# Kernel optimization log

Measured on AMD Instinct MI355X. Metric: run time of the kernel, lower is better.

## Reference

```python
import jax, jax.numpy as jnp
import numpy as np
from jax import lax

B, DIM, H, W = 8, 192, 128, 128
HEADS = 4
CH = DIM // HEADS            # per-head channels = 48
D_RED = max(DIM // 8, 4)     # SKFusion reduction dim = 24
HEIGHT = 2


def setup_inputs() -> dict:
    key = jax.random.key(0)
    ks = jax.random.split(key, 32)
    rn = lambda i, shp, s=1.0: jax.random.normal(ks[i], shp, jnp.float32) * s
    inp = {
        "T_E_input": rn(0, (B, DIM, H, W)),
        "C_E_input": rn(1, (B, DIM, H, W)),
        "T_D_input": rn(2, (B, DIM, H, W)),
        # LayerNorm2d params
        "tn_w": jnp.ones((DIM,), jnp.float32), "tn_b": jnp.zeros((DIM,), jnp.float32),
        "cn_w": jnp.ones((DIM,), jnp.float32), "cn_b": jnp.zeros((DIM,), jnp.float32),
        # Q/K/V: 1x1 conv [O,C] + depthwise 3x3 [DIM,1,3,3]
        "q_w": rn(3, (DIM, DIM), 0.05), "q_b": jnp.zeros((DIM,), jnp.float32),
        "q_dw": rn(4, (DIM, 1, 3, 3), 0.05), "q_db": jnp.zeros((DIM,), jnp.float32),
        "k_w": rn(5, (DIM, DIM), 0.05), "k_b": jnp.zeros((DIM,), jnp.float32),
        "k_dw": rn(6, (DIM, 1, 3, 3), 0.05), "k_db": jnp.zeros((DIM,), jnp.float32),
        "v_w": rn(7, (DIM, DIM), 0.05), "v_b": jnp.zeros((DIM,), jnp.float32),
        "v_dw": rn(8, (DIM, 1, 3, 3), 0.05), "v_db": jnp.zeros((DIM,), jnp.float32),
        "temperature": jnp.ones((1, 1, 1), jnp.float32),
        "proj_w": rn(9, (DIM, DIM), 0.05), "proj_b": jnp.zeros((DIM,), jnp.float32),
        "a1": jnp.full((1,), 0.2, jnp.float32),
        "a2": jnp.full((1,), 0.2, jnp.float32),
        "a3": jnp.full((1,), 0.2, jnp.float32),
        "a4": jnp.full((1,), 0.2, jnp.float32),
        # SKFusion mlp (both conv 1x1, no bias)
        "sk_w1": rn(10, (D_RED, DIM), 0.05),
        "sk_w2": rn(11, (DIM * HEIGHT, D_RED), 0.05),
    }
    return inp


def _ln2d(x, w, b, eps=1e-6):
    mu = x.mean(axis=1, keepdims=True)
    var = x.var(axis=1, keepdims=True)
    return (x - mu) / jnp.sqrt(var + eps) * w[None, :, None, None] + b[None, :, None, None]


def _conv1x1(x, w, b=None):
    y = jnp.einsum('bchw,oc->bohw', x, w)
    return y if b is None else y + b[None, :, None, None]


def _dwconv3x3(x, w, b):
    y = lax.conv_general_dilated(x, w, (1, 1), 'SAME',
                                 feature_group_count=DIM,
                                 dimension_numbers=('NCHW', 'OIHW', 'NCHW'))
    return y + b[None, :, None, None]


def _l2norm(x, eps=1e-12):
    n = jnp.sqrt(jnp.sum(x * x, axis=-1, keepdims=True))
    return x / jnp.maximum(n, eps)


def _topk_masked(attn, k):
    # mask built from top-k indices via scatter (one-hot over last axis)
    idx = lax.top_k(attn, k)[1]                              # [b,h,C,k]
    mask = jax.nn.one_hot(idx, attn.shape[-1], dtype=bool).any(axis=-2)
    return jnp.where(mask, attn, -jnp.inf)


def _gfm_forward(T_E_input, C_E_input, T_D_input,
                 tn_w, tn_b, cn_w, cn_b,
                 q_w, q_b, q_dw, q_db,
                 k_w, k_b, k_dw, k_db,
                 v_w, v_b, v_dw, v_db,
                 temperature, proj_w, proj_b,
                 a1, a2, a3, a4, sk_w1, sk_w2):
    b, c, h, w = T_E_input.shape
    T_E = _ln2d(T_E_input, tn_w, tn_b)
    C_E = _ln2d(C_E_input, cn_w, cn_b)

    q = _dwconv3x3(_conv1x1(T_E, q_w, q_b), q_dw, q_db)
    k = _dwconv3x3(_conv1x1(C_E, k_w, k_b), k_dw, k_db)
    v = _dwconv3x3(_conv1x1(C_E, v_w, v_b), v_dw, v_db)

    hw = h * w
    q = _l2norm(q.reshape(b, HEADS, CH, hw))   # normalize along token dim
    k = _l2norm(k.reshape(b, HEADS, CH, hw))
    v = v.reshape(b, HEADS, CH, hw)

    attn = jnp.einsum('bhcn,bhdn->bhcd', q, k) * temperature  # [b,h,C,C]

    C = CH
    ks = [C // 2, C * 2 // 3, int(C * 3 / 4), int(C * 4 / 5)]
    p1 = jax.nn.softmax(_topk_masked(attn, ks[0]), axis=-1)
    p2 = jax.nn.softmax(_topk_masked(attn, ks[1]), axis=-1)
    p3 = jax.nn.softmax(_topk_masked(attn, ks[2]), axis=-1)
    p4 = jax.nn.softmax(_topk_masked(attn, ks[3]), axis=-1)

    o1 = jnp.einsum('bhcd,bhdn->bhcn', p1, v)
    o2 = jnp.einsum('bhcd,bhdn->bhcn', p2, v)
    o3 = jnp.einsum('bhcd,bhdn->bhcn', p3, v)
    o4 = jnp.einsum('bhcd,bhdn->bhcn', p4, v)
    out = o1 * a1 + o2 * a2 + o3 * a3 + o4 * a4

    fusion1 = _conv1x1(out.reshape(b, c, h, w), proj_w, proj_b) + C_E_input

    # SKFusion over [fusion1, T_D_input]
    feats = jnp.stack([fusion1, T_D_input], axis=1)          # [b,2,c,h,w]
    feats_sum = feats.sum(axis=1)                            # [b,c,h,w]
    pooled = feats_sum.mean(axis=(2, 3), keepdims=True)      # [b,c,1,1]
    z = jax.nn.relu(_conv1x1(pooled, sk_w1))
    gate = _conv1x1(z, sk_w2).reshape(b, HEIGHT, c, 1, 1)
    gate = jax.nn.softmax(gate, axis=1)
    return (feats * gate).sum(axis=1)


def reference(T_E_input, C_E_input, T_D_input,
              tn_w, tn_b, cn_w, cn_b,
              q_w, q_b, q_dw, q_db,
              k_w, k_b, k_dw, k_db,
              v_w, v_b, v_dw, v_db,
              temperature, proj_w, proj_b,
              a1, a2, a3, a4, sk_w1, sk_w2):
    return _gfm_forward(T_E_input, C_E_input, T_D_input,
                        tn_w, tn_b, cn_w, cn_b,
                        q_w, q_b, q_dw, q_db,
                        k_w, k_b, k_dw, k_db,
                        v_w, v_b, v_dw, v_db,
                        temperature, proj_w, proj_b,
                        a1, a2, a3, a4, sk_w1, sk_w2)
```

## Files before the change

### kernel.cpp

```cpp
#include <hip/hip_runtime.h>
#include <hip/hip_bf16.h>

#define BATCH 8
#define CDIM 192
#define HH 128
#define WW 128
#define HW (HH*WW)
#define HEADS 4
#define CHD 48
#define NSL 64
#define LDK 40

typedef __attribute__((ext_vector_type(8))) short bf16x8;
typedef __attribute__((ext_vector_type(4))) float f32x4;

__device__ inline unsigned short f2bf(float f) {
    union { float f; unsigned int u; } v; v.f = f;
    unsigned int u = v.u;
    unsigned int r = u + 0x7fff + ((u >> 16) & 1);
    return (unsigned short)(r >> 16);
}

__global__ __launch_bounds__(256) void ln_part_kernel(
    const float* __restrict__ x, float* __restrict__ ps, float* __restrict__ ps2)
{
    const int idx = blockIdx.x * 256 + threadIdx.x;
    const int slice = blockIdx.y;
    const int b = idx >> 14;
    const int p = idx & (HW - 1);
    const float* xp = x + (size_t)b * CDIM * HW + (size_t)slice * 48 * HW + p;
    float s = 0.f, s2 = 0.f;
#pragma unroll 8
    for (int c = 0; c < 48; ++c) {
        float v = xp[(size_t)c * HW];
        s += v;
        s2 = fmaf(v, v, s2);
    }
    ps [slice * (BATCH * HW) + idx] = s;
    ps2[slice * (BATCH * HW) + idx] = s2;
}

__global__ __launch_bounds__(256) void ln_fin_kernel(
    const float* __restrict__ ps, const float* __restrict__ ps2,
    float* __restrict__ mu, float* __restrict__ rstd)
{
    const int idx = blockIdx.x * 256 + threadIdx.x;
    const int N = BATCH * HW;
    float s  = ps [idx] + ps [N + idx] + ps [2 * N + idx] + ps [3 * N + idx];
    float s2 = ps2[idx] + ps2[N + idx] + ps2[2 * N + idx] + ps2[3 * N + idx];
    float m = s * (1.f / CDIM);
    mu[idx] = m;
    rstd[idx] = rsqrtf(s2 * (1.f / CDIM) - m * m + 1e-6f);
}

__global__ __launch_bounds__(256) void rowsum_kernel(
    const float* __restrict__ x, float* __restrict__ out)
{
    const int row = blockIdx.x;
    const float4* xp = (const float4*)(x + (size_t)row * HW);
    float s = 0.f;
#pragma unroll
    for (int k = 0; k < 16; ++k) {
        float4 v = xp[threadIdx.x + k * 256];
        s += (v.x + v.y) + (v.z + v.w);
    }
    for (int msk = 32; msk; msk >>= 1) s += __shfl_xor(s, msk);
    __shared__ float sh[4];
    if ((threadIdx.x & 63) == 0) sh[threadIdx.x >> 6] = s;
    __syncthreads();
    if (threadIdx.x == 0) out[row] = sh[0] + sh[1] + sh[2] + sh[3];
}

__global__ __launch_bounds__(256) void conv1x1_mfma_ln(
    const float* __restrict__ x, const float* __restrict__ mu, const float* __restrict__ rstd,
    const float* __restrict__ lnw, const float* __restrict__ lnb,
    const float* __restrict__ w, const float* __restrict__ wb,
    float* __restrict__ y)
{
    __shared__ short A_s[CDIM * LDK];
    __shared__ short B_s[64 * LDK];
    const int tid = threadIdx.x;
    const int p0 = blockIdx.x * 64;
    const int b  = blockIdx.y;
    const int lane = tid & 63;
    const int wid = tid >> 6;
    const int p_l = tid & 63;

    const int sidx = (b << 14) + p0 + p_l;
    const float m_ln = mu[sidx], r_ln = rstd[sidx];

    f32x4 acc[12];
#pragma unroll
    for (int i = 0; i < 12; ++i) acc[i] = f32x4{0.f, 0.f, 0.f, 0.f};

    const size_t xb = (size_t)b * CDIM * HW + p0;

    for (int ks = 0; ks < 6; ++ks) {
        const int k0 = ks * 32;
        if (ks) __syncthreads();
#pragma unroll
        for (int j = 0; j < 3; ++j) {
            const int row = p_l + 64 * j;
#pragma unroll
            for (int i = 0; i < 2; ++i) {
                const int c = k0 + wid * 8 + i * 4;
                const float4 wv = *(const float4*)(w + (size_t)row * CDIM + c);
                unsigned int lo = f2bf(wv.x) | ((unsigned int)f2bf(wv.y) << 16);
                unsigned int hi = f2bf(wv.z) | ((unsigned int)f2bf(wv.w) << 16);
                *(uint2*)&A_s[row * LDK + wid * 8 + i * 4] = make_uint2(lo, hi);
            }
        }
#pragma unroll
        for (int i = 0; i < 2; ++i) {
            const int c = k0 + wid * 8 + i * 4;
            float v0 = x[xb + (size_t)(c + 0) * HW + p_l];
            float v1 = x[xb + (size_t)(c + 1) * HW + p_l];
            float v2 = x[xb + (size_t)(c + 2) * HW + p_l];
            float v3 = x[xb + (size_t)(c + 3) * HW + p_l];
            v0 = (v0 - m_ln) * r_ln * lnw[c + 0] + lnb[c + 0];
            v1 = (v1 - m_ln) * r_ln * lnw[c + 1] + lnb[c + 1];
            v2 = (v2 - m_ln) * r_ln * lnw[c + 2] + lnb[c + 2];
            v3 = (v3 - m_ln) * r_ln * lnw[c + 3] + lnb[c + 3];
            unsigned int lo = f2bf(v0) | ((unsigned int)f2bf(v1) << 16);
            unsigned int hi = f2bf(v2) | ((unsigned int)f2bf(v3) << 16);
            *(uint2*)&B_s[p_l * LDK + wid * 8 + i * 4] = make_uint2(lo, hi);
        }
        __syncthreads();
        const bf16x8 bfr = *(const bf16x8*)&B_s[(wid * 16 + (lane & 15)) * LDK + (lane >> 4) * 8];
#pragma unroll
        for (int mi = 0; mi < 12; ++mi) {
            const bf16x8 afr = *(const bf16x8*)&A_s[(mi * 16 + (lane & 15)) * LDK + (lane >> 4) * 8];
            acc[mi] = __builtin_amdgcn_mfma_f32_16x16x32_bf16(afr, bfr, acc[mi], 0, 0, 0);
        }
    }
    const int col = p0 + wid * 16 + (lane & 15);
#pragma unroll
    for (int mi = 0; mi < 12; ++mi) {
#pragma unroll
        for (int r = 0; r < 4; ++r) {
            const int row = mi * 16 + (lane >> 4) * 4 + r;
            y[((size_t)b * CDIM + row) * HW + col] = acc[mi][r] + wb[row];
        }
    }
}

__global__ __launch_bounds__(256) void projfuse_mfma(
    const float* __restrict__ v, const float* __restrict__ M,
    const float* __restrict__ pb, const float* __restrict__ resid,
    float* __restrict__ y)
{
    __shared__ short A_s[CDIM * LDK];
    __shared__ short B_s[64 * LDK];
    const int tid = threadIdx.x;
    const int p0 = blockIdx.x * 64;
    const int b  = blockIdx.y;
    const int lane = tid & 63;
    const int wid = tid >> 6;
    const int p_l = tid & 63;

    f32x4 acc[12];
#pragma unroll
    for (int i = 0; i < 12; ++i) acc[i] = f32x4{0.f, 0.f, 0.f, 0.f};

    const size_t xb = (size_t)b * CDIM * HW + p0;
    const float* Mb = M + (size_t)b * CDIM * CDIM;

    for (int ks = 0; ks < 6; ++ks) {
        const int k0 = ks * 32;
        if (ks) __syncthreads();
#pragma unroll
        for (int j = 0; j < 3; ++j) {
            const int row = p_l + 64 * j;
#pragma unroll
            for (int i = 0; i < 2; ++i) {
                const int c = k0 + wid * 8 + i * 4;
                const float4 wv = *(const float4*)(Mb + (size_t)row * CDIM + c);
                unsigned int lo = f2bf(wv.x) | ((unsigned int)f2bf(wv.y) << 16);
                unsigned int hi = f2bf(wv.z) | ((unsigned int)f2bf(wv.w) << 16);
                *(uint2*)&A_s[row * LDK + wid * 8 + i * 4] = make_uint2(lo, hi);
            }
        }
#pragma unroll
        for (int i = 0; i < 2; ++i) {
            const int c = k0 + wid * 8 + i * 4;
            float v0 = v[xb + (size_t)(c + 0) * HW + p_l];
            float v1 = v[xb + (size_t)(c + 1) * HW + p_l];
            float v2 = v[xb + (size_t)(c + 2) * HW + p_l];
            float v3 = v[xb + (size_t)(c + 3) * HW + p_l];
            unsigned int lo = f2bf(v0) | ((unsigned int)f2bf(v1) << 16);
            unsigned int hi = f2bf(v2) | ((unsigned int)f2bf(v3) << 16);
            *(uint2*)&B_s[p_l * LDK + wid * 8 + i * 4] = make_uint2(lo, hi);
        }
        __syncthreads();
        const bf16x8 bfr = *(const bf16x8*)&B_s[(wid * 16 + (lane & 15)) * LDK + (lane >> 4) * 8];
#pragma unroll
        for (int mi = 0; mi < 12; ++mi) {
            const bf16x8 afr = *(const bf16x8*)&A_s[(mi * 16 + (lane & 15)) * LDK + (lane >> 4) * 8];
            acc[mi] = __builtin_amdgcn_mfma_f32_16x16x32_bf16(afr, bfr, acc[mi], 0, 0, 0);
        }
    }
    const int col = p0 + wid * 16 + (lane & 15);
#pragma unroll
    for (int mi = 0; mi < 12; ++mi) {
#pragma unroll
        for (int r = 0; r < 4; ++r) {
            const int row = mi * 16 + (lane >> 4) * 4 + r;
            const size_t o = ((size_t)b * CDIM + row) * HW + col;
            y[o] = acc[mi][r] + pb[row] + resid[o];
        }
    }
}

__global__ __launch_bounds__(256) void dwconv_kernel(
    const float* __restrict__ x, const float* __restrict__ w, const float* __restrict__ bias,
    float* __restrict__ y, float* __restrict__ sumsq)
{
    const int rt = blockIdx.x, c = blockIdx.y, b = blockIdx.z;
    const int tid = threadIdx.x;
    const int lrow = tid >> 3;
    const int c16  = (tid & 7) * 16;
    const int gr = rt * 32 + lrow;
    const float* xp = x + ((size_t)b * CDIM + c) * HW;

    float wv[9];
#pragma unroll
    for (int t = 0; t < 9; ++t) wv[t] = w[c * 9 + t];
    const float bs = bias[c];

    float rb[3][24];
#pragma unroll
    for (int dr = 0; dr < 3; ++dr) {
        const int grr = gr + dr - 1;
        const bool ok = (grr >= 0) && (grr < HH);
        const float4* rp = (const float4*)(xp + (size_t)(ok ? grr : 0) * WW);
        float4 z = make_float4(0.f, 0.f, 0.f, 0.f);
        float4 t0 = (ok && c16 > 0)        ? rp[(c16 >> 2) - 1] : z;
        float4 t1 = ok ? rp[(c16 >> 2) + 0] : z;
        float4 t2 = ok ? rp[(c16 >> 2) + 1] : z;
        float4 t3 = ok ? rp[(c16 >> 2) + 2] : z;
        float4 t4 = ok ? rp[(c16 >> 2) + 3] : z;
        float4 t5 = (ok && c16 + 16 < WW)  ? rp[(c16 >> 2) + 4] : z;
        *(float4*)&rb[dr][0]  = t0;
        *(float4*)&rb[dr][4]  = t1;
        *(float4*)&rb[dr][8]  = t2;
        *(float4*)&rb[dr][12] = t3;
        *(float4*)&rb[dr][16] = t4;
        *(float4*)&rb[dr][20] = t5;
    }

    float out[16];
#pragma unroll
    for (int p = 0; p < 16; ++p) out[p] = bs;
#pragma unroll
    for (int dr = 0; dr < 3; ++dr) {
#pragma unroll
        for (int p = 0; p < 16; ++p) {
            out[p] = fmaf(wv[dr * 3 + 0], rb[dr][3 + p], out[p]);
            out[p] = fmaf(wv[dr * 3 + 1], rb[dr][4 + p], out[p]);
            out[p] = fmaf(wv[dr * 3 + 2], rb[dr][5 + p], out[p]);
        }
    }

    float* yp = y + ((size_t)b * CDIM + c) * HW + (size_t)gr * WW + c16;
#pragma unroll
    for (int q = 0; q < 4; ++q)
        ((float4*)yp)[q] = make_float4(out[4*q], out[4*q+1], out[4*q+2], out[4*q+3]);

    if (sumsq != nullptr) {
        float ss = 0.f;
#pragma unroll
        for (int p = 0; p < 16; ++p) ss = fmaf(out[p], out[p], ss);
        for (int msk = 32; msk; msk >>= 1) ss += __shfl_xor(ss, msk);
        __shared__ float sh[4];
        if ((tid & 63) == 0) sh[tid >> 6] = ss;
        __syncthreads();
        if (tid == 0) atomicAdd(&sumsq[b * CDIM + c], sh[0] + sh[1] + sh[2] + sh[3]);
    }
}

__global__ __launch_bounds__(256) void attn_kernel(
    const float* __restrict__ q, const float* __restrict__ k, float* __restrict__ attn)
{
    const int bh = blockIdx.y;
    const int b = bh >> 2, h = bh & 3;
    const int n0 = blockIdx.x * (HW / NSL);
    __shared__ float qs[48][65];
    __shared__ float ks[48][65];
    const int tid = threadIdx.x;
    const int c0 = (tid >> 4) * 3, d0 = (tid & 15) * 3;
    float s[3][3] = {{0.f,0.f,0.f},{0.f,0.f,0.f},{0.f,0.f,0.f}};
    const size_t qbase = ((size_t)b * CDIM + h * CHD) * HW;
    for (int ch = 0; ch < HW / NSL; ch += 64) {
        __syncthreads();
        for (int idx = tid; idx < 48 * 64; idx += 256) {
            int r = idx >> 6, col = idx & 63;
            qs[r][col] = q[qbase + (size_t)r * HW + n0 + ch + col];
            ks[r][col] = k[qbase + (size_t)r * HW + n0 + ch + col];
        }
        __syncthreads();
        for (int n = 0; n < 64; ++n) {
            float qv[3], kv[3];
#pragma unroll
            for (int t = 0; t < 3; ++t) { qv[t] = qs[c0 + t][n]; kv[t] = ks[d0 + t][n]; }
#pragma unroll
            for (int a = 0; a < 3; ++a)
#pragma unroll
                for (int e = 0; e < 3; ++e) s[a][e] = fmaf(qv[a], kv[e], s[a][e]);
        }
    }
    float* ap = attn + (size_t)bh * 48 * 48;
#pragma unroll
    for (int a = 0; a < 3; ++a)
#pragma unroll
        for (int e = 0; e < 3; ++e) atomicAdd(&ap[(c0 + a) * 48 + (d0 + e)], s[a][e]);
}

__global__ __launch_bounds__(64) void peff_kernel(
    const float* __restrict__ attn, const float* __restrict__ rq2, const float* __restrict__ rk2,
    const float* __restrict__ temp,
    const float* __restrict__ a1, const float* __restrict__ a2,
    const float* __restrict__ a3, const float* __restrict__ a4,
    float* __restrict__ peff)
{
    __shared__ float a_sh[48][64];
    __shared__ float e_sh[48][64];
    __shared__ float c_sh[48][64];
    const int t = threadIdx.x;
    const int r = blockIdx.x * 64 + t;
    const int bh = r / 48, c = r - bh * 48;
    const int b = bh >> 2, h = bh & 3;
    const float T = temp[0];
    const float nq = sqrtf(rq2[b * CDIM + h * CHD + c]);
    const float scq = 1.f / fmaxf(nq, 1e-12f);
    float m = -1e30f;
    for (int d = 0; d < 48; ++d) {
        float nk = sqrtf(rk2[b * CDIM + h * CHD + d]);
        float a = attn[(size_t)r * 48 + d] * scq * (1.f / fmaxf(nk, 1e-12f)) * T;
        a_sh[d][t] = a;
        m = fmaxf(m, a);
    }
    float S1 = 0.f, S2 = 0.f, S3 = 0.f, S4 = 0.f;
    for (int d = 0; d < 48; ++d) {
        float ad = a_sh[d][t];
        int cnt = 0;
        for (int e = 0; e < 48; ++e) cnt += (a_sh[e][t] > ad) ? 1 : 0;
        float ed = expf(ad - m);
        e_sh[d][t] = ed;
        c_sh[d][t] = (float)cnt;
        if (cnt < 24) S1 += ed;
        if (cnt < 32) S2 += ed;
        if (cnt < 36) S3 += ed;
        if (cnt < 38) S4 += ed;
    }
    float w1 = a1[0] / S1, w2 = a2[0] / S2, w3 = a3[0] / S3, w4 = a4[0] / S4;
    for (int d = 0; d < 48; ++d) {
        float ed = e_sh[d][t];
        int cnt = (int)c_sh[d][t];
        float pw = 0.f;
        if (cnt < 24) pw += w1;
        if (cnt < 32) pw += w2;
        if (cnt < 36) pw += w3;
        if (cnt < 38) pw += w4;
        peff[(size_t)r * 48 + d] = ed * pw;
    }
}

__global__ __launch_bounds__(192) void mmat_kernel(
    const float* __restrict__ peff, const float* __restrict__ pw, float* __restrict__ M)
{
    const int b = blockIdx.x, h = blockIdx.y, o = threadIdx.x;
    __shared__ float pf[48 * 48];
    for (int i = o; i < 48 * 48; i += 192) pf[i] = peff[(size_t)(b * HEADS + h) * 2304 + i];
    __syncthreads();
    float pwr[48];
#pragma unroll
    for (int cc = 0; cc < 48; ++cc) pwr[cc] = pw[o * CDIM + h * CHD + cc];
    float* Mo = M + ((size_t)b * CDIM + o) * CDIM + h * CHD;
    for (int d = 0; d < 48; ++d) {
        float s = 0.f;
#pragma unroll
        for (int cc = 0; cc < 48; ++cc) s = fmaf(pwr[cc], pf[cc * 48 + d], s);
        Mo[d] = s;
    }
}

__global__ __launch_bounds__(192) void gate_kernel(
    const float* __restrict__ sum_f1, const float* __restrict__ sum_td,
    const float* __restrict__ w1, const float* __restrict__ w2, float* __restrict__ gates)
{
    const int b = blockIdx.x;
    const int t = threadIdx.x;
    __shared__ float pooled[192];
    __shared__ float z[24];
    pooled[t] = (sum_f1[b * CDIM + t] + sum_td[b * CDIM + t]) * (1.f / HW);
    __syncthreads();
    if (t < 24) {
        float s = 0.f;
        for (int c2 = 0; c2 < CDIM; ++c2) s += w1[t * CDIM + c2] * pooled[c2];
        z[t] = fmaxf(s, 0.f);
    }
    __syncthreads();
    float g0 = 0.f, g1 = 0.f;
    for (int j = 0; j < 24; ++j) {
        g0 += w2[t * 24 + j] * z[j];
        g1 += w2[(CDIM + t) * 24 + j] * z[j];
    }
    float mm = fmaxf(g0, g1);
    float e0 = expf(g0 - mm), e1 = expf(g1 - mm);
    float inv = 1.f / (e0 + e1);
    gates[b * CDIM + t] = e0 * inv;
    gates[BATCH * CDIM + b * CDIM + t] = e1 * inv;
}

__global__ __launch_bounds__(256) void final_kernel(
    const float* __restrict__ f1, const float* __restrict__ td,
    const float* __restrict__ gates, float* __restrict__ out)
{
    size_t i4 = (size_t)blockIdx.x * 256 + threadIdx.x;
    size_t i = i4 * 4;
    int plane = (int)(i / HW);
    float g0 = gates[plane], g1 = gates[BATCH * CDIM + plane];
    float4 a = ((const float4*)f1)[i4];
    float4 d = ((const float4*)td)[i4];
    float4 r;
    r.x = a.x * g0 + d.x * g1;
    r.y = a.y * g0 + d.y * g1;
    r.z = a.z * g0 + d.z * g1;
    r.w = a.w * g0 + d.w * g1;
    ((float4*)out)[i4] = r;
}

extern "C" void kernel_launch(void* const* d_in, const int* in_sizes, int n_in,
                              void* d_out, int out_size, void* d_ws, size_t ws_size,
                              hipStream_t stream)
{
    const float* T_E  = (const float*)d_in[0];
    const float* C_E  = (const float*)d_in[1];
    const float* T_D  = (const float*)d_in[2];
    const float* tn_w = (const float*)d_in[3];
    const float* tn_b = (const float*)d_in[4];
    const float* cn_w = (const float*)d_in[5];
    const float* cn_b = (const float*)d_in[6];
    const float* q_w  = (const float*)d_in[7];
    const float* q_b  = (const float*)d_in[8];
    const float* q_dw = (const float*)d_in[9];
    const float* q_db = (const float*)d_in[10];
    const float* k_w  = (const float*)d_in[11];
    const float* k_b  = (const float*)d_in[12];
    const float* k_dw = (const float*)d_in[13];
    const float* k_db = (const float*)d_in[14];
    const float* v_w  = (const float*)d_in[15];
    const float* v_b  = (const float*)d_in[16];
    const float* v_dw = (const float*)d_in[17];
    const float* v_db = (const float*)d_in[18];
    const float* temp = (const float*)d_in[19];
    const float* p_w  = (const float*)d_in[20];
    const float* p_b  = (const float*)d_in[21];
    const float* a1   = (const float*)d_in[22];
    const float* a2   = (const float*)d_in[23];
    const float* a3   = (const float*)d_in[24];
    const float* a4   = (const float*)d_in[25];
    const float* skw1 = (const float*)d_in[26];
    const float* skw2 = (const float*)d_in[27];

    float* ws = (float*)d_ws;
    float* rq2    = ws;
    float* rk2    = rq2 + 1536;
    float* sum_td = rk2 + 1536;
    float* sum_f1 = sum_td + 1536;
    float* attn   = sum_f1 + 1536;
    float* peff   = attn + 73728;
    float* gates  = peff + 73728;
    float* Mmat   = gates + 3072;
    float* muT    = Mmat + 294912;
    float* rsT    = muT + 131072;
    float* muC    = rsT + 131072;
    float* rsC    = muC + 131072;

    const size_t BIG = (size_t)BATCH * CDIM * HW;
    float* bufA = ws + (1 << 20);
    float* bufB = bufA + BIG;
    float* bufC = bufB + BIG;
    float* lps  = bufC;
    float* lps2 = bufC + 524288;
    float* outF = (float*)d_out;

    hipMemsetAsync(ws, 0, (size_t)79872 * sizeof(float), stream);

    dim3 lgrid(512, 4);
    ln_part_kernel<<<lgrid, 256, 0, stream>>>(T_E, lps, lps2);
    ln_fin_kernel<<<512, 256, 0, stream>>>(lps, lps2, muT, rsT);
    ln_part_kernel<<<lgrid, 256, 0, stream>>>(C_E, lps, lps2);
    ln_fin_kernel<<<512, 256, 0, stream>>>(lps, lps2, muC, rsC);
    rowsum_kernel<<<BATCH * CDIM, 256, 0, stream>>>(T_D, sum_td);

    dim3 ggrid(HW / 64, BATCH);
    conv1x1_mfma_ln<<<ggrid, 256, 0, stream>>>(T_E, muT, rsT, tn_w, tn_b, q_w, q_b, bufA);
    conv1x1_mfma_ln<<<ggrid, 256, 0, stream>>>(C_E, muC, rsC, cn_w, cn_b, k_w, k_b, bufB);
    conv1x1_mfma_ln<<<ggrid, 256, 0, stream>>>(C_E, muC, rsC, cn_w, cn_b, v_w, v_b, bufC);

    dim3 dgrid(HH / 32, CDIM, BATCH);
    dwconv_kernel<<<dgrid, 256, 0, stream>>>(bufA, q_dw, q_db, outF, rq2);
    dwconv_kernel<<<dgrid, 256, 0, stream>>>(bufB, k_dw, k_db, bufA, rk2);
    dwconv_kernel<<<dgrid, 256, 0, stream>>>(bufC, v_dw, v_db, bufB, nullptr);

    attn_kernel<<<dim3(NSL, BATCH * HEADS), 256, 0, stream>>>(outF, bufA, attn);
    peff_kernel<<<24, 64, 0, stream>>>(attn, rq2, rk2, temp, a1, a2, a3, a4, peff);
    mmat_kernel<<<dim3(BATCH, HEADS), 192, 0, stream>>>(peff, p_w, Mmat);

    projfuse_mfma<<<ggrid, 256, 0, stream>>>(bufB, Mmat, p_b, C_E, bufC);
    rowsum_kernel<<<BATCH * CDIM, 256, 0, stream>>>(bufC, sum_f1);

    gate_kernel<<<BATCH, 192, 0, stream>>>(sum_f1, sum_td, skw1, skw2, gates);
    final_kernel<<<(BIG / 4) / 256, 256, 0, stream>>>(bufC, T_D, gates, outF);
}
```

Before: 1.164 ms.

## Pre-convert weights to bf16 and hold weight fragments in registers for 1x1 GEMMs

Adds a kernel that converts the q/k/v weights to bf16 once, and has mmat_kernel write M directly in bf16. The 1x1 conv and projection GEMM kernels now load each wave's 48-row slice of weights straight into registers as MFMA fragments, instead of converting the whole fp32 weight matrix into shared memory on every k-step in every block. Each wave now covers 48 output rows by 64 pixels rather than 192 by 16. This removes redundant weight conversion and LDS traffic per block, at the cost of higher register pressure (18 bf16x8 A fragments plus 12 accumulators per lane).

```diff
diff --git a/kernel.cpp b/kernel.cpp
--- a/kernel.cpp
+++ b/kernel.cpp
@@ -19,6 +19,18 @@
     unsigned int u = v.u;
     unsigned int r = u + 0x7fff + ((u >> 16) & 1);
     return (unsigned short)(r >> 16);
+}
+
+__global__ __launch_bounds__(256) void wcvt_kernel(
+    const float* __restrict__ qw, const float* __restrict__ kw, const float* __restrict__ vw,
+    unsigned short* __restrict__ qb, unsigned short* __restrict__ kb, unsigned short* __restrict__ vb)
+{
+    const int i = blockIdx.x * 256 + threadIdx.x;
+    if (i < CDIM * CDIM) {
+        qb[i] = f2bf(qw[i]);
+        kb[i] = f2bf(kw[i]);
+        vb[i] = f2bf(vw[i]);
+    }
 }
 
 __global__ __launch_bounds__(256) void ln_part_kernel(
@@ -74,10 +86,9 @@
 __global__ __launch_bounds__(256) void conv1x1_mfma_ln(
     const float* __restrict__ x, const float* __restrict__ mu, const float* __restrict__ rstd,
     const float* __restrict__ lnw, const float* __restrict__ lnb,
-    const float* __restrict__ w, const float* __restrict__ wb,
+    const unsigned short* __restrict__ wbf, const float* __restrict__ wb,
     float* __restrict__ y)
 {
-    __shared__ short A_s[CDIM * LDK];
     __shared__ short B_s[64 * LDK];
     const int tid = threadIdx.x;
     const int p0 = blockIdx.x * 64;
@@ -85,31 +96,32 @@
     const int lane = tid & 63;
     const int wid = tid >> 6;
     const int p_l = tid & 63;
+    const int m0 = wid * 48;
+
+    bf16x8 afr[3][6];
+#pragma unroll
+    for (int mi = 0; mi < 3; ++mi)
+#pragma unroll
+        for (int ks = 0; ks < 6; ++ks) {
+            const int row = m0 + mi * 16 + (lane & 15);
+            const int k   = ks * 32 + (lane >> 4) * 8;
+            afr[mi][ks] = *(const bf16x8*)&wbf[row * CDIM + k];
+        }
 
     const int sidx = (b << 14) + p0 + p_l;
     const float m_ln = mu[sidx], r_ln = rstd[sidx];
 
-    f32x4 acc[12];
-#pragma unroll
-    for (int i = 0; i < 12; ++i) acc[i] = f32x4{0.f, 0.f, 0.f, 0.f};
+    f32x4 acc[3][4];
+#pragma unroll
+    for (int mi = 0; mi < 3; ++mi)
+#pragma unroll
+        for (int nf = 0; nf < 4; ++nf) acc[mi][nf] = f32x4{0.f, 0.f, 0.f, 0.f};
 
     const size_t xb = (size_t)b * CDIM * HW + p0;
 
     for (int ks = 0; ks < 6; ++ks) {
         const int k0 = ks * 32;
         if (ks) __syncthreads();
-#pragma unroll
-        for (int j = 0; j < 3; ++j) {
-            const int row = p_l + 64 * j;
-#pragma unroll
-            for (int i = 0; i < 2; ++i) {
-                const int c = k0 + wid * 8 + i * 4;
-                const float4 wv = *(const float4*)(w + (size_t)row * CDIM + c);
-                unsigned int lo = f2bf(wv.x) | ((unsigned int)f2bf(wv.y) << 16);
-                unsigned int hi = f2bf(wv.z) | ((unsigned int)f2bf(wv.w) << 16);
-                *(uint2*)&A_s[row * LDK + wid * 8 + i * 4] = make_uint2(lo, hi);
-            }
-        }
 #pragma unroll
         for (int i = 0; i < 2; ++i) {
             const int c = k0 + wid * 8 + i * 4;
@@ -126,30 +138,34 @@
             *(uint2*)&B_s[p_l * LDK + wid * 8 + i * 4] = make_uint2(lo, hi);
         }
         __syncthreads();
-        const bf16x8 bfr = *(const bf16x8*)&B_s[(wid * 16 + (lane & 15)) * LDK + (lane >> 4) * 8];
-#pragma unroll
-        for (int mi = 0; mi < 12; ++mi) {
-            const bf16x8 afr = *(const bf16x8*)&A_s[(mi * 16 + (lane & 15)) * LDK + (lane >> 4) * 8];
-            acc[mi] = __builtin_amdgcn_mfma_f32_16x16x32_bf16(afr, bfr, acc[mi], 0, 0, 0);
-        }
-    }
-    const int col = p0 + wid * 16 + (lane & 15);
-#pragma unroll
-    for (int mi = 0; mi < 12; ++mi) {
-#pragma unroll
-        for (int r = 0; r < 4; ++r) {
-            const int row = mi * 16 + (lane >> 4) * 4 + r;
-            y[((size_t)b * CDIM + row) * HW + col] = acc[mi][r] + wb[row];
-        }
-    }
+        bf16x8 bfr[4];
+#pragma unroll
+        for (int nf = 0; nf < 4; ++nf)
+            bfr[nf] = *(const bf16x8*)&B_s[(nf * 16 + (lane & 15)) * LDK + (lane >> 4) * 8];
+#pragma unroll
+        for (int mi = 0; mi < 3; ++mi)
+#pragma unroll
+            for (int nf = 0; nf < 4; ++nf)
+                acc[mi][nf] = __builtin_amdgcn_mfma_f32_16x16x32_bf16(afr[mi][ks], bfr[nf], acc[mi][nf], 0, 0, 0);
+    }
+#pragma unroll
+    for (int mi = 0; mi < 3; ++mi)
+#pragma unroll
+        for (int nf = 0; nf < 4; ++nf) {
+            const int col = p0 + nf * 16 + (lane & 15);
+#pragma unroll
+            for (int r = 0; r < 4; ++r) {
+                const int row = m0 + mi * 16 + (lane >> 4) * 4 + r;
+                y[((size_t)b * CDIM + row) * HW + col] = acc[mi][nf][r] + wb[row];
+            }
+        }
 }
 
 __global__ __launch_bounds__(256) void projfuse_mfma(
-    const float* __restrict__ v, const float* __restrict__ M,
+    const float* __restrict__ v, const unsigned short* __restrict__ Mb,
     const float* __restrict__ pb, const float* __restrict__ resid,
     float* __restrict__ y)
 {
-    __shared__ short A_s[CDIM * LDK];
     __shared__ short B_s[64 * LDK];
     const int tid = threadIdx.x;
     const int p0 = blockIdx.x * 64;
@@ -157,29 +173,30 @@
     const int lane = tid & 63;
     const int wid = tid >> 6;
     const int p_l = tid & 63;
-
-    f32x4 acc[12];
-#pragma unroll
-    for (int i = 0; i < 12; ++i) acc[i] = f32x4{0.f, 0.f, 0.f, 0.f};
+    const int m0 = wid * 48;
+
+    const unsigned short* Mw = Mb + (size_t)b * CDIM * CDIM;
+    bf16x8 afr[3][6];
+#pragma unroll
+    for (int mi = 0; mi < 3; ++mi)
+#pragma unroll
+        for (int ks = 0; ks < 6; ++ks) {
+            const int row = m0 + mi * 16 + (lane & 15);
+            const int k   = ks * 32 + (lane >> 4) * 8;
+            afr[mi][ks] = *(const bf16x8*)&Mw[row * CDIM + k];
+        }
+
+    f32x4 acc[3][4];
+#pragma unroll
+    for (int mi = 0; mi < 3; ++mi)
+#pragma unroll
+        for (int nf = 0; nf < 4; ++nf) acc[mi][nf] = f32x4{0.f, 0.f, 0.f, 0.f};
 
     const size_t xb = (size_t)b * CDIM * HW + p0;
-    const float* Mb = M + (size_t)b * CDIM * CDIM;
 
     for (int ks = 0; ks < 6; ++ks) {
         const int k0 = ks * 32;
         if (ks) __syncthreads();
-#pragma unroll
-        for (int j = 0; j < 3; ++j) {
-            const int row = p_l + 64 * j;
-#pragma unroll
-            for (int i = 0; i < 2; ++i) {
-                const int c = k0 + wid * 8 + i * 4;
-                const float4 wv = *(const float4*)(Mb + (size_t)row * CDIM + c);
-                unsigned int lo = f2bf(wv.x) | ((unsigned int)f2bf(wv.y) << 16);
-                unsigned int hi = f2bf(wv.z) | ((unsigned int)f2bf(wv.w) << 16);
-                *(uint2*)&A_s[row * LDK + wid * 8 + i * 4] = make_uint2(lo, hi);
-            }
-        }
 #pragma unroll
         for (int i = 0; i < 2; ++i) {
             const int c = k0 + wid * 8 + i * 4;
@@ -192,23 +209,28 @@
             *(uint2*)&B_s[p_l * LDK + wid * 8 + i * 4] = make_uint2(lo, hi);
         }
         __syncthreads();
-        const bf16x8 bfr = *(const bf16x8*)&B_s[(wid * 16 + (lane & 15)) * LDK + (lane >> 4) * 8];
-#pragma unroll
-        for (int mi = 0; mi < 12; ++mi) {
-            const bf16x8 afr = *(const bf16x8*)&A_s[(mi * 16 + (lane & 15)) * LDK + (lane >> 4) * 8];
-            acc[mi] = __builtin_amdgcn_mfma_f32_16x16x32_bf16(afr, bfr, acc[mi], 0, 0, 0);
-        }
-    }
-    const int col = p0 + wid * 16 + (lane & 15);
-#pragma unroll
-    for (int mi = 0; mi < 12; ++mi) {
-#pragma unroll
-        for (int r = 0; r < 4; ++r) {
-            const int row = mi * 16 + (lane >> 4) * 4 + r;
-            const size_t o = ((size_t)b * CDIM + row) * HW + col;
-            y[o] = acc[mi][r] + pb[row] + resid[o];
-        }
-    }
+        bf16x8 bfr[4];
+#pragma unroll
+        for (int nf = 0; nf < 4; ++nf)
+            bfr[nf] = *(const bf16x8*)&B_s[(nf * 16 + (lane & 15)) * LDK + (lane >> 4) * 8];
+#pragma unroll
+        for (int mi = 0; mi < 3; ++mi)
+#pragma unroll
+            for (int nf = 0; nf < 4; ++nf)
+                acc[mi][nf] = __builtin_amdgcn_mfma_f32_16x16x32_bf16(afr[mi][ks], bfr[nf], acc[mi][nf], 0, 0, 0);
+    }
+#pragma unroll
+    for (int mi = 0; mi < 3; ++mi)
+#pragma unroll
+        for (int nf = 0; nf < 4; ++nf) {
+            const int col = p0 + nf * 16 + (lane & 15);
+#pragma unroll
+            for (int r = 0; r < 4; ++r) {
+                const int row = m0 + mi * 16 + (lane >> 4) * 4 + r;
+                const size_t o = ((size_t)b * CDIM + row) * HW + col;
+                y[o] = acc[mi][nf][r] + pb[row] + resid[o];
+            }
+        }
 }
 
 __global__ __launch_bounds__(256) void dwconv_kernel(
@@ -366,7 +388,7 @@
 }
 
 __global__ __launch_bounds__(192) void mmat_kernel(
-    const float* __restrict__ peff, const float* __restrict__ pw, float* __restrict__ M)
+    const float* __restrict__ peff, const float* __restrict__ pw, unsigned short* __restrict__ Mb)
 {
     const int b = blockIdx.x, h = blockIdx.y, o = threadIdx.x;
     __shared__ float pf[48 * 48];
@@ -375,12 +397,12 @@
     float pwr[48];
 #pragma unroll
     for (int cc = 0; cc < 48; ++cc) pwr[cc] = pw[o * CDIM + h * CHD + cc];
-    float* Mo = M + ((size_t)b * CDIM + o) * CDIM + h * CHD;
+    unsigned short* Mo = Mb + ((size_t)b * CDIM + o) * CDIM + h * CHD;
     for (int d = 0; d < 48; ++d) {
         float s = 0.f;
 #pragma unroll
         for (int cc = 0; cc < 48; ++cc) s = fmaf(pwr[cc], pf[cc * 48 + d], s);
-        Mo[d] = s;
+        Mo[d] = f2bf(s);
     }
 }
 
@@ -471,11 +493,14 @@
     float* attn   = sum_f1 + 1536;
     float* peff   = attn + 73728;
     float* gates  = peff + 73728;
-    float* Mmat   = gates + 3072;
-    float* muT    = Mmat + 294912;
+    float* muT    = gates + 3072;
     float* rsT    = muT + 131072;
     float* muC    = rsT + 131072;
     float* rsC    = muC + 131072;
+    unsigned short* wqb = (unsigned short*)(rsC + 131072);
+    unsigned short* wkb = wqb + CDIM * CDIM;
+    unsigned short* wvb = wkb + CDIM * CDIM;
+    unsigned short* Mb  = wvb + CDIM * CDIM;
 
     const size_t BIG = (size_t)BATCH * CDIM * HW;
     float* bufA = ws + (1 << 20);
@@ -487,6 +512,8 @@
 
     hipMemsetAsync(ws, 0, (size_t)79872 * sizeof(float), stream);
 
+    wcvt_kernel<<<(CDIM * CDIM + 255) / 256, 256, 0, stream>>>(q_w, k_w, v_w, wqb, wkb, wvb);
+
     dim3 lgrid(512, 4);
     ln_part_kernel<<<lgrid, 256, 0, stream>>>(T_E, lps, lps2);
     ln_fin_kernel<<<512, 256, 0, stream>>>(lps, lps2, muT, rsT);
@@ -495,9 +522,9 @@
     rowsum_kernel<<<BATCH * CDIM, 256, 0, stream>>>(T_D, sum_td);
 
     dim3 ggrid(HW / 64, BATCH);
-    conv1x1_mfma_ln<<<ggrid, 256, 0, stream>>>(T_E, muT, rsT, tn_w, tn_b, q_w, q_b, bufA);
-    conv1x1_mfma_ln<<<ggrid, 256, 0, stream>>>(C_E, muC, rsC, cn_w, cn_b, k_w, k_b, bufB);
-    conv1x1_mfma_ln<<<ggrid, 256, 0, stream>>>(C_E, muC, rsC, cn_w, cn_b, v_w, v_b, bufC);
+    conv1x1_mfma_ln<<<ggrid, 256, 0, stream>>>(T_E, muT, rsT, tn_w, tn_b, wqb, q_b, bufA);
+    conv1x1_mfma_ln<<<ggrid, 256, 0, stream>>>(C_E, muC, rsC, cn_w, cn_b, wkb, k_b, bufB);
+    conv1x1_mfma_ln<<<ggrid, 256, 0, stream>>>(C_E, muC, rsC, cn_w, cn_b, wvb, v_b, bufC);
 
     dim3 dgrid(HH / 32, CDIM, BATCH);
     dwconv_kernel<<<dgrid, 256, 0, stream>>>(bufA, q_dw, q_db, outF, rq2);
@@ -506,9 +533,9 @@
 
     attn_kernel<<<dim3(NSL, BATCH * HEADS), 256, 0, stream>>>(outF, bufA, attn);
     peff_kernel<<<24, 64, 0, stream>>>(attn, rq2, rk2, temp, a1, a2, a3, a4, peff);
-    mmat_kernel<<<dim3(BATCH, HEADS), 192, 0, stream>>>(peff, p_w, Mmat);
-
-    projfuse_mfma<<<ggrid, 256, 0, stream>>>(bufB, Mmat, p_b, C_E, bufC);
+    mmat_kernel<<<dim3(BATCH, HEADS), 192, 0, stream>>>(peff, p_w, Mb);
+
+    projfuse_mfma<<<ggrid, 256, 0, stream>>>(bufB, Mb, p_b, C_E, bufC);
     rowsum_kernel<<<BATCH * CDIM, 256, 0, stream>>>(bufC, sum_f1);
 
     gate_kernel<<<BATCH, 192, 0, stream>>>(sum_f1, sum_td, skw1, skw2, gates);
```

Measured after the change: 1.059 ms. 1.1x faster.
